# Optimization experiments

Hardware: AMD Instinct MI355X
Metric: run time of the kernel (lower is better)

## Reference

```python
import jax, jax.numpy as jnp
import numpy as np

HIDDEN = 512
HEADS = 8
HEAD_DIM = HIDDEN // HEADS
THRESH = 0.1
EPS = 1e-8


def setup_inputs() -> dict:
    key = jax.random.key(0)
    ks = jax.random.split(key, 9)
    B, S = 2, 4096
    scale = 1.0 / np.sqrt(HIDDEN)
    x = jax.random.normal(ks[0], (B, S, HIDDEN), dtype=jnp.float32)
    Wq = jax.random.normal(ks[1], (HIDDEN, HIDDEN), dtype=jnp.float32) * scale
    bq = jnp.zeros((HIDDEN,), dtype=jnp.float32)
    Wk = jax.random.normal(ks[2], (HIDDEN, HIDDEN), dtype=jnp.float32) * scale
    bk = jnp.zeros((HIDDEN,), dtype=jnp.float32)
    Wv = jax.random.normal(ks[3], (HIDDEN, HIDDEN), dtype=jnp.float32) * scale
    bv = jnp.zeros((HIDDEN,), dtype=jnp.float32)
    Wo = jax.random.normal(ks[4], (HIDDEN, HIDDEN), dtype=jnp.float32) * scale
    bo = jnp.zeros((HIDDEN,), dtype=jnp.float32)
    return {"x": x, "Wq": Wq, "bq": bq, "Wk": Wk, "bk": bk,
            "Wv": Wv, "bv": bv, "Wo": Wo, "bo": bo}


def reference(x, Wq, bq, Wk, bk, Wv, bv, Wo, bo):
    B, S, _ = x.shape
    # torch Linear: y = x @ W.T + b
    def proj(W, b):
        y = jnp.einsum('bsd,ed->bse', x, W) + b
        return y.reshape(B, S, HEADS, HEAD_DIM).transpose(0, 2, 1, 3)  # [B,H,S,Dh]
    Q = proj(Wq, bq)
    K = proj(Wk, bk)
    V = proj(Wv, bv)
    scores = jnp.einsum('bhqd,bhkd->bhqk', Q, K) / jnp.sqrt(jnp.float32(HEAD_DIM))
    probs = jax.nn.softmax(scores, axis=-1)  # [B,H,S,S]
    probs = jnp.where(probs > THRESH, probs, 0.0)
    probs = probs / (jnp.sum(probs, axis=-1, keepdims=True) + EPS)
    ctx = jnp.einsum('bhqk,bhkd->bhqd', probs, V)
    ctx = ctx.transpose(0, 2, 1, 3).reshape(B, S, HIDDEN)
    return jnp.einsum('bsd,ed->bse', ctx, Wo) + bo
```

## Files before the change

### kernel.cpp

```cpp
#include <hip/hip_runtime.h>

#define S_LEN 4096
#define BATCH 2
#define HID 512
#define HEADS 8
#define HD 64
#define NX (BATCH * S_LEN * HID)
#define WSZ (HID * HID)
#define NBH (BATCH * HEADS)
#define QB 32
#define NB1 (S_LEN / QB * NBH)
#define NB2 (S_LEN / 64 * NBH)

typedef short v8s __attribute__((ext_vector_type(8)));
typedef float v4f __attribute__((ext_vector_type(4)));
typedef float v16f __attribute__((ext_vector_type(16)));
typedef unsigned short ushort_t;

__device__ __forceinline__ ushort_t f2bf(float f) {
  unsigned u = __builtin_bit_cast(unsigned, f);
  u += 0x7fffu + ((u >> 16) & 1u);
  return (ushort_t)(u >> 16);
}
__device__ __forceinline__ unsigned pk2(float a, float b) {
  return (__builtin_bit_cast(unsigned, a) >> 16) |
         (__builtin_bit_cast(unsigned, b) & 0xFFFF0000u);
}
__device__ __forceinline__ float fexp2(float x) {
  return __builtin_amdgcn_exp2f(x);
}


__global__ __launch_bounds__(256) void cvt_k(
    const float* __restrict__ x,
    const float* __restrict__ wq, const float* __restrict__ wk,
    const float* __restrict__ wv, const float* __restrict__ wo,
    ushort_t* __restrict__ dst)
{
  const size_t e = ((size_t)blockIdx.x * 256 + threadIdx.x) * 4;
  const float* src; size_t off;
  if (e < NX) { src = x; off = e; }
  else {
    const size_t we = e - NX;
    const int wi = (int)(we >> 18);
    src = wi == 0 ? wq : wi == 1 ? wk : wi == 2 ? wv : wo;
    off = we & (WSZ - 1);
  }
  float4 v = *(const float4*)&src[off];
  uint2 u; u.x = pk2(v.x, v.y); u.y = pk2(v.z, v.w);
  *(uint2*)&dst[e] = u;
}

__global__ __launch_bounds__(256) void gemm_qkv(
    const ushort_t* __restrict__ X, const ushort_t* __restrict__ Wb,
    const float* __restrict__ bq, const float* __restrict__ bk, const float* __restrict__ bv,
    ushort_t* __restrict__ Qf, ushort_t* __restrict__ Kf, ushort_t* __restrict__ Vw,
    float qscale)
{
  __shared__ ushort_t As[128][40];
  __shared__ ushort_t Bs[128][40];
  const int t = threadIdx.x;
  const int lane = t & 63;
  const int l15 = lane & 15, lg = lane >> 4;
  const int w = t >> 6;
  const int wr = w >> 1, wc = w & 1;
  const int m0 = blockIdx.y * 128;
  const int wsel = blockIdx.x >> 2;
  const int e0 = (blockIdx.x & 3) * 128;
  const ushort_t* W = Wb + (size_t)wsel * WSZ;
  const float* bias = wsel == 0 ? bq : wsel == 1 ? bk : bv;
  const float osc = (wsel == 0) ? qscale : 1.0f;

  v4f acc[4][4] = {};
  const int srow = t >> 2, scol = (t & 3) * 8;

  for (int k0 = 0; k0 < HID; k0 += 32) {
    __syncthreads();
    #pragma unroll
    for (int rep = 0; rep < 2; ++rep) {
      *(uint4*)&As[srow + rep * 64][scol] =
          *(const uint4*)&X[(size_t)(m0 + srow + rep * 64) * HID + k0 + scol];
      *(uint4*)&Bs[srow + rep * 64][scol] =
          *(const uint4*)&W[(size_t)(e0 + srow + rep * 64) * HID + k0 + scol];
    }
    __syncthreads();
    v8s a[4], b[4];
    #pragma unroll
    for (int fr = 0; fr < 4; ++fr)
      a[fr] = *(const v8s*)&As[wr * 64 + 16 * fr + l15][8 * lg];
    #pragma unroll
    for (int fc = 0; fc < 4; ++fc)
      b[fc] = *(const v8s*)&Bs[wc * 64 + 16 * fc + l15][8 * lg];
    #pragma unroll
    for (int fr = 0; fr < 4; ++fr)
      #pragma unroll
      for (int fc = 0; fc < 4; ++fc)
        acc[fr][fc] = __builtin_amdgcn_mfma_f32_16x16x32_bf16(a[fr], b[fc], acc[fr][fc], 0, 0, 0);
  }

  #pragma unroll
  for (int fr = 0; fr < 4; ++fr)
    #pragma unroll
    for (int fc = 0; fc < 4; ++fc) {
      const int e = e0 + wc * 64 + 16 * fc + l15;
      const float bval = bias[e];
      #pragma unroll
      for (int r = 0; r < 4; ++r) {
        const int m = m0 + wr * 64 + 16 * fr + 4 * lg + r;
        const float v = (acc[fr][fc][r] + bval) * osc;
        const int bidx = m >> 12, s = m & (S_LEN - 1);
        const int hh = e >> 6, dh = e & 63;
        const size_t hb = ((size_t)(bidx * HEADS + hh)) * (size_t)(S_LEN * HD);
        if (wsel == 2) {
          Vw[hb + (size_t)s * HD + dh] = f2bf(v);
        } else {
          const size_t off = (size_t)(s >> 5) * 2048 +
              (size_t)(((dh >> 4) * 64 + ((dh >> 3) & 1) * 32 + (s & 31)) * 8 + (dh & 7));
          (wsel == 0 ? Qf : Kf)[hb + off] = f2bf(v);
        }
      }
    }
}

__global__ __launch_bounds__(256, 4) void attn_p1(
    const ushort_t* __restrict__ Qf, const ushort_t* __restrict__ Kf,
    ushort_t* __restrict__ Cb, int* __restrict__ Flg)
{
  __shared__ float RedL[4][QB];
  __shared__ float RedM[4][QB];
  __shared__ int bflag;
  const int t = threadIdx.x;
  const int lane = t & 63;
  const int l31 = lane & 31, hi = lane >> 5;
  const int kq = t >> 6;
  const int lin = blockIdx.x;
  const int bh = ((lin & 7) << 1) | ((lin >> 3) & 1);
  const int q0 = (lin >> 4) * QB;
  if (t == 0) bflag = 0;

  const size_t hoff = (size_t)bh * (size_t)(S_LEN * HD);
  const ushort_t* Qb = Qf + hoff + (size_t)(q0 >> 5) * 2048;
  const ushort_t* Kb = Kf + hoff;

  v8s qa[4];
  #pragma unroll
  for (int ks = 0; ks < 4; ++ks)
    qa[ks] = *(const v8s*)&Qb[(ks * 64 + lane) * 8];

  float M[16], L[16];
  #pragma unroll
  for (int j = 0; j < 16; ++j) { M[j] = -1e30f; L[j] = 0.f; }

  v8s kA[4], kB4[4];
  {
    const ushort_t* kc = Kb + (size_t)kq * 2048;
    #pragma unroll
    for (int ks = 0; ks < 4; ++ks)
      kA[ks] = *(const v8s*)&kc[(ks * 64 + lane) * 8];
  }

#define PROC(KX)                                                            \
  {                                                                         \
    v16f s = {};                                                            \
    _Pragma("unroll")                                                       \
    for (int ks = 0; ks < 4; ++ks)                                          \
      s = __builtin_amdgcn_mfma_f32_32x32x16_bf16(qa[ks], KX[ks], s, 0, 0, 0); \
    _Pragma("unroll")                                                       \
    for (int j = 0; j < 16; ++j) {                                          \
      M[j] = fmaxf(M[j], s[j]);                                             \
      L[j] += fexp2(s[j]);                                                  \
    }                                                                       \
  }

  for (int i = 0; i < 32; i += 2) {
    {
      const ushort_t* kc = Kb + (size_t)(kq + 4 * (i + 1)) * 2048;
      #pragma unroll
      for (int ks = 0; ks < 4; ++ks)
        kB4[ks] = *(const v8s*)&kc[(ks * 64 + lane) * 8];
    }
    PROC(kA)
    {
      const int c2 = (i + 2 < 32) ? (kq + 4 * (i + 2)) : kq;
      const ushort_t* kc = Kb + (size_t)c2 * 2048;
      #pragma unroll
      for (int ks = 0; ks < 4; ++ks)
        kA[ks] = *(const v8s*)&kc[(ks * 64 + lane) * 8];
    }
    PROC(kB4)
  }
#undef PROC

  #pragma unroll
  for (int j = 0; j < 16; ++j) {
    float Lv = L[j], Mv = M[j];
    Lv += __shfl_xor(Lv, 1);  Mv = fmaxf(Mv, __shfl_xor(Mv, 1));
    Lv += __shfl_xor(Lv, 2);  Mv = fmaxf(Mv, __shfl_xor(Mv, 2));
    Lv += __shfl_xor(Lv, 4);  Mv = fmaxf(Mv, __shfl_xor(Mv, 4));
    Lv += __shfl_xor(Lv, 8);  Mv = fmaxf(Mv, __shfl_xor(Mv, 8));
    Lv += __shfl_xor(Lv, 16); Mv = fmaxf(Mv, __shfl_xor(Mv, 16));
    if (l31 == 0) {
      const int row = (j & 3) + 8 * (j >> 2) + 4 * hi;
      RedL[kq][row] = Lv;
      RedM[kq][row] = Mv;
    }
  }
  __syncthreads();
  if (t < QB) {
    const float Lv = RedL[0][t] + RedL[1][t] + RedL[2][t] + RedL[3][t];
    const float Mv = fmaxf(fmaxf(RedM[0][t], RedM[1][t]),
                           fmaxf(RedM[2][t], RedM[3][t]));
    if (Mv >= __log2f(Lv) - 3.3719281f) atomicOr(&bflag, 1);
  }
  __syncthreads();
  if (t == 0) Flg[lin] = bflag;

  const int b = bh >> 3, h = bh & 7;
  const int row = t >> 3, d8 = (t & 7) * 8;
  const uint4 z = {0u, 0u, 0u, 0u};
  *(uint4*)&Cb[((size_t)b * S_LEN + q0 + row) * HID + h * HD + d8] = z;
}

__global__ __launch_bounds__(256) void attn_p2(
    const ushort_t* __restrict__ Qf, const ushort_t* __restrict__ Kf,
    const ushort_t* __restrict__ V, ushort_t* __restrict__ Cb,
    const int* __restrict__ Flg)
{
  const int lin = blockIdx.x;
  {
    const int base = lin & 15, qb = lin >> 4;
    if ((Flg[base | ((2 * qb) << 4)] | Flg[base | ((2 * qb + 1) << 4)]) == 0)
      return;
  }
  __shared__ float Osh[64][HD + 1];
  __shared__ float Dsh[64];
  __shared__ float RedA[4][64];
  __shared__ float iLs[64];
  __shared__ ushort_t Pp[4][32][40];
  __shared__ ushort_t VT[4][HD][40];
  const int t = threadIdx.x;
  const int lane = t & 63;
  const int l31 = lane & 31, hi = lane >> 5;
  const int w = t >> 6;
  const int bh = ((lin & 7) << 1) | ((lin >> 3) & 1);
  const int q0 = (lin >> 4) * 64;
  const size_t hoff = (size_t)bh * (size_t)(S_LEN * HD);
  const ushort_t* Qb = Qf + hoff + (size_t)(q0 >> 5) * 2048;
  const ushort_t* Kb = Kf + hoff;
  const ushort_t* Vh = V + hoff;

  if (t < 64) Dsh[t] = 0.f;
  for (int idx = t; idx < 64 * HD; idx += 256) Osh[idx >> 6][idx & 63] = 0.f;

  v8s qa[4], qB[4];
  #pragma unroll
  for (int ks = 0; ks < 4; ++ks) {
    qa[ks] = *(const v8s*)&Qb[(ks * 64 + lane) * 8];
    qB[ks] = *(const v8s*)&Qb[2048 + (ks * 64 + lane) * 8];
  }

  float L0[16], L1[16];
  #pragma unroll
  for (int j = 0; j < 16; ++j) { L0[j] = 0.f; L1[j] = 0.f; }
  for (int i = 0; i < 32; ++i) {
    const ushort_t* kc = Kb + (size_t)(w + 4 * i) * 2048;
    v8s kb[4];
    #pragma unroll
    for (int ks = 0; ks < 4; ++ks)
      kb[ks] = *(const v8s*)&kc[(ks * 64 + lane) * 8];
    v16f sa = {}, sb = {};
    #pragma unroll
    for (int ks = 0; ks < 4; ++ks) {
      sa = __builtin_amdgcn_mfma_f32_32x32x16_bf16(qa[ks], kb[ks], sa, 0, 0, 0);
      sb = __builtin_amdgcn_mfma_f32_32x32x16_bf16(qB[ks], kb[ks], sb, 0, 0, 0);
    }
    #pragma unroll
    for (int j = 0; j < 16; ++j) {
      L0[j] += fexp2(sa[j]);
      L1[j] += fexp2(sb[j]);
    }
  }
  #pragma unroll
  for (int rseti = 0; rseti < 2; ++rseti)
    #pragma unroll
    for (int j = 0; j < 16; ++j) {
      float Lv = (rseti == 0) ? L0[j] : L1[j];
      Lv += __shfl_xor(Lv, 1);  Lv += __shfl_xor(Lv, 2);
      Lv += __shfl_xor(Lv, 4);  Lv += __shfl_xor(Lv, 8);
      Lv += __shfl_xor(Lv, 16);
      if (l31 == 0) {
        const int row = rseti * 32 + (j & 3) + 8 * (j >> 2) + 4 * hi;
        RedA[w][row] = Lv;
      }
    }
  __syncthreads();
  if (t < 64)
    iLs[t] = 1.0f / (RedA[0][t] + RedA[1][t] + RedA[2][t] + RedA[3][t]);
  __syncthreads();

  float il[2][16];
  #pragma unroll
  for (int rseti = 0; rseti < 2; ++rseti)
    #pragma unroll
    for (int j = 0; j < 16; ++j)
      il[rseti][j] = iLs[rseti * 32 + (j & 3) + 8 * (j >> 2) + 4 * hi];

  v16f oA[2] = {}, oB[2] = {};
  float den[2][16] = {};

  for (int i = 0; i < 32; ++i) {
    const int c = w + 4 * i;
    const ushort_t* kc = Kb + (size_t)c * 2048;
    v8s kb[4];
    #pragma unroll
    for (int ks = 0; ks < 4; ++ks)
      kb[ks] = *(const v8s*)&kc[(ks * 64 + lane) * 8];
    v16f sa = {}, sb = {};
    #pragma unroll
    for (int ks = 0; ks < 4; ++ks) {
      sa = __builtin_amdgcn_mfma_f32_32x32x16_bf16(qa[ks], kb[ks], sa, 0, 0, 0);
      sb = __builtin_amdgcn_mfma_f32_32x32x16_bf16(qB[ks], kb[ks], sb, 0, 0, 0);
    }
    {
      const ushort_t* vsrc = &Vh[((size_t)c * 32 + l31) * HD + hi * 32];
      #pragma unroll
      for (int qq = 0; qq < 4; ++qq) {
        uint4 vv = *(const uint4*)&vsrc[qq * 8];
        const ushort_t* pv = (const ushort_t*)&vv;
        #pragma unroll
        for (int jj = 0; jj < 8; ++jj)
          VT[w][hi * 32 + qq * 8 + jj][l31] = pv[jj];
      }
    }
    #pragma unroll
    for (int rseti = 0; rseti < 2; ++rseti) {
      #pragma unroll
      for (int j = 0; j < 16; ++j) {
        const float s = (rseti == 0) ? sa[j] : sb[j];
        const int row = (j & 3) + 8 * (j >> 2) + 4 * hi;
        float p = fexp2(s) * il[rseti][j];
        p = (p > 0.1f) ? p : 0.f;
        den[rseti][j] += p;
        Pp[w][row][l31] = f2bf(p);
      }
      v8s pa0 = *(const v8s*)&Pp[w][l31][8 * hi];
      v8s pa1 = *(const v8s*)&Pp[w][l31][16 + 8 * hi];
      #pragma unroll
      for (int dblk = 0; dblk < 2; ++dblk) {
        v8s vb0 = *(const v8s*)&VT[w][dblk * 32 + l31][8 * hi];
        v8s vb1 = *(const v8s*)&VT[w][dblk * 32 + l31][16 + 8 * hi];
        if (rseti == 0) {
          oA[dblk] = __builtin_amdgcn_mfma_f32_32x32x16_bf16(pa0, vb0, oA[dblk], 0, 0, 0);
          oA[dblk] = __builtin_amdgcn_mfma_f32_32x32x16_bf16(pa1, vb1, oA[dblk], 0, 0, 0);
        } else {
          oB[dblk] = __builtin_amdgcn_mfma_f32_32x32x16_bf16(pa0, vb0, oB[dblk], 0, 0, 0);
          oB[dblk] = __builtin_amdgcn_mfma_f32_32x32x16_bf16(pa1, vb1, oB[dblk], 0, 0, 0);
        }
      }
    }
  }

  #pragma unroll
  for (int rseti = 0; rseti < 2; ++rseti)
    #pragma unroll
    for (int j = 0; j < 16; ++j) {
      float d = den[rseti][j];
      d += __shfl_xor(d, 1); d += __shfl_xor(d, 2); d += __shfl_xor(d, 4);
      d += __shfl_xor(d, 8); d += __shfl_xor(d, 16);
      const int row = rseti * 32 + (j & 3) + 8 * (j >> 2) + 4 * hi;
      if (l31 == 0) atomicAdd(&Dsh[row], d);
    }
  #pragma unroll
  for (int rseti = 0; rseti < 2; ++rseti)
    #pragma unroll
    for (int dblk = 0; dblk < 2; ++dblk)
      #pragma unroll
      for (int j = 0; j < 16; ++j) {
        const int row = rseti * 32 + (j & 3) + 8 * (j >> 2) + 4 * hi;
        const float val = (rseti == 0) ? oA[dblk][j] : oB[dblk][j];
        atomicAdd(&Osh[row][dblk * 32 + l31], val);
      }
  __syncthreads();
  const int b = bh >> 3, h = bh & 7;
  for (int idx = t; idx < 64 * HD; idx += 256) {
    const int row = idx >> 6, d = idx & 63;
    const float val = Osh[row][d] / (Dsh[row] + 1e-8f);
    Cb[((size_t)b * S_LEN + q0 + row) * HID + h * HD + d] = f2bf(val);
  }
}

__global__ __launch_bounds__(256) void gemm_out(
    const ushort_t* __restrict__ X, const ushort_t* __restrict__ W,
    const float* __restrict__ bias, const int* __restrict__ Flg,
    float* __restrict__ Df)
{
  const int t = threadIdx.x;
  const int m0 = blockIdx.y * 64;
  const int e0 = blockIdx.x * 64;

  {
    const int b = m0 >> 12, qblk = (m0 & (S_LEN - 1)) >> 6;
    int any = 0;
    #pragma unroll
    for (int h = 0; h < HEADS; ++h) {
      const int bhh = b * HEADS + h;
      const int base = (bhh >> 1) | ((bhh & 1) << 3);
      any |= Flg[base | ((2 * qblk) << 4)] | Flg[base | ((2 * qblk + 1) << 4)];
    }
    if (!any) {
      const int row = t >> 2, c0 = (t & 3) * 16;
      #pragma unroll
      for (int g = 0; g < 4; ++g) {
        const float4 bv = *(const float4*)&bias[e0 + c0 + g * 4];
        *(float4*)&Df[(size_t)(m0 + row) * HID + e0 + c0 + g * 4] = bv;
      }
      return;
    }
  }

  __shared__ ushort_t As[64][40];
  __shared__ ushort_t Bs[64][40];
  const int lane = t & 63;
  const int l15 = lane & 15, lg = lane >> 4;
  const int w = t >> 6;
  const int wr = w >> 1, wc = w & 1;

  v4f acc[2][2] = {};
  const int srow = t >> 2, scol = (t & 3) * 8;

  for (int k0 = 0; k0 < HID; k0 += 32) {
    __syncthreads();
    *(uint4*)&As[srow][scol] =
        *(const uint4*)&X[(size_t)(m0 + srow) * HID + k0 + scol];
    *(uint4*)&Bs[srow][scol] =
        *(const uint4*)&W[(size_t)(e0 + srow) * HID + k0 + scol];
    __syncthreads();
    v8s a[2], b[2];
    #pragma unroll
    for (int fr = 0; fr < 2; ++fr)
      a[fr] = *(const v8s*)&As[wr * 32 + 16 * fr + l15][8 * lg];
    #pragma unroll
    for (int fc = 0; fc < 2; ++fc)
      b[fc] = *(const v8s*)&Bs[wc * 32 + 16 * fc + l15][8 * lg];
    #pragma unroll
    for (int fr = 0; fr < 2; ++fr)
      #pragma unroll
      for (int fc = 0; fc < 2; ++fc)
        acc[fr][fc] = __builtin_amdgcn_mfma_f32_16x16x32_bf16(a[fr], b[fc], acc[fr][fc], 0, 0, 0);
  }

  #pragma unroll
  for (int fr = 0; fr < 2; ++fr)
    #pragma unroll
    for (int fc = 0; fc < 2; ++fc) {
      const int e = e0 + wc * 32 + 16 * fc + l15;
      const float bval = bias[e];
      #pragma unroll
      for (int r = 0; r < 4; ++r) {
        const int m = m0 + wr * 32 + 16 * fr + 4 * lg + r;
        Df[(size_t)m * HID + e] = acc[fr][fc][r] + bval;
      }
    }
}

extern "C" void kernel_launch(void* const* d_in, const int* in_sizes, int n_in,
                              void* d_out, int out_size, void* d_ws, size_t ws_size,
                              hipStream_t stream) {
  const float* x  = (const float*)d_in[0];
  const float* Wq = (const float*)d_in[1];
  const float* bq = (const float*)d_in[2];
  const float* Wk = (const float*)d_in[3];
  const float* bk = (const float*)d_in[4];
  const float* Wv = (const float*)d_in[5];
  const float* bv = (const float*)d_in[6];
  const float* Wo = (const float*)d_in[7];
  const float* bo = (const float*)d_in[8];

  int*      Flg  = (int*)d_ws;
  ushort_t* xb   = (ushort_t*)(Flg + NB1);
  ushort_t* wqb  = xb + NX;
  ushort_t* wob  = wqb + 3 * WSZ;
  ushort_t* Qf   = wob + WSZ;
  ushort_t* Kf   = Qf + NX;
  ushort_t* Vw   = Kf + NX;
  ushort_t* Cb   = Vw + NX;

  const float qscale = 0.125f * 1.44269504f;

  cvt_k<<<(NX + 4 * WSZ) / 1024, 256, 0, stream>>>(x, Wq, Wk, Wv, Wo, xb);

  gemm_qkv<<<dim3(12, 64), 256, 0, stream>>>(
      xb, wqb, bq, bk, bv, Qf, Kf, Vw, qscale);

  attn_p1<<<NB1, 256, 0, stream>>>(Qf, Kf, Cb, Flg);
  attn_p2<<<NB2, 256, 0, stream>>>(Qf, Kf, Vw, Cb, Flg);

  gemm_out<<<dim3(8, 128), 256, 0, stream>>>(Cb, wob, bo, Flg, (float*)d_out);
}
```

Baseline: 105.7 us.

## Use direct global-to-LDS loads, triple-buffer K loads, and skip zeroing context

The QKV GEMM now stages tiles with global_load_lds straight into unpadded shared arrays instead of going through registers. attn_p1 triple-buffers K fragments, raises wave priority around the MFMA block, and no longer zeroes the context buffer. gemm_out instead substitutes zeros for head slices whose flags are off, so it never reads unwritten context. Risks are LDS bank conflicts from dropping the padding and correctness depending on the flag mask matching each 64-wide head slice.

```diff
diff --git a/kernel.cpp b/kernel.cpp
--- a/kernel.cpp
+++ b/kernel.cpp
@@ -16,6 +16,8 @@
 typedef float v4f __attribute__((ext_vector_type(4)));
 typedef float v16f __attribute__((ext_vector_type(16)));
 typedef unsigned short ushort_t;
+typedef const __attribute__((address_space(1))) unsigned gu32;
+typedef __attribute__((address_space(3))) unsigned lu32;
 
 __device__ __forceinline__ ushort_t f2bf(float f) {
   unsigned u = __builtin_bit_cast(unsigned, f);
@@ -57,8 +59,8 @@
     ushort_t* __restrict__ Qf, ushort_t* __restrict__ Kf, ushort_t* __restrict__ Vw,
     float qscale)
 {
-  __shared__ ushort_t As[128][40];
-  __shared__ ushort_t Bs[128][40];
+  __shared__ ushort_t As[128][32];
+  __shared__ ushort_t Bs[128][32];
   const int t = threadIdx.x;
   const int lane = t & 63;
   const int l15 = lane & 15, lg = lane >> 4;
@@ -72,17 +74,22 @@
   const float osc = (wsel == 0) ? qscale : 1.0f;
 
   v4f acc[4][4] = {};
-  const int srow = t >> 2, scol = (t & 3) * 8;
+  const int r0 = t >> 2, c0 = (t & 3) * 8;
 
   for (int k0 = 0; k0 < HID; k0 += 32) {
     __syncthreads();
-    #pragma unroll
-    for (int rep = 0; rep < 2; ++rep) {
-      *(uint4*)&As[srow + rep * 64][scol] =
-          *(const uint4*)&X[(size_t)(m0 + srow + rep * 64) * HID + k0 + scol];
-      *(uint4*)&Bs[srow + rep * 64][scol] =
-          *(const uint4*)&W[(size_t)(e0 + srow + rep * 64) * HID + k0 + scol];
-    }
+    __builtin_amdgcn_global_load_lds(
+        (gu32*)(const void*)&X[(size_t)(m0 + r0) * HID + k0 + c0],
+        (lu32*)(void*)&As[r0][c0], 16, 0, 0);
+    __builtin_amdgcn_global_load_lds(
+        (gu32*)(const void*)&X[(size_t)(m0 + r0 + 64) * HID + k0 + c0],
+        (lu32*)(void*)&As[r0 + 64][c0], 16, 0, 0);
+    __builtin_amdgcn_global_load_lds(
+        (gu32*)(const void*)&W[(size_t)(e0 + r0) * HID + k0 + c0],
+        (lu32*)(void*)&Bs[r0][c0], 16, 0, 0);
+    __builtin_amdgcn_global_load_lds(
+        (gu32*)(const void*)&W[(size_t)(e0 + r0 + 64) * HID + k0 + c0],
+        (lu32*)(void*)&Bs[r0 + 64][c0], 16, 0, 0);
     __syncthreads();
     v8s a[4], b[4];
     #pragma unroll
@@ -124,7 +131,7 @@
 
 __global__ __launch_bounds__(256, 4) void attn_p1(
     const ushort_t* __restrict__ Qf, const ushort_t* __restrict__ Kf,
-    ushort_t* __restrict__ Cb, int* __restrict__ Flg)
+    int* __restrict__ Flg)
 {
   __shared__ float RedL[4][QB];
   __shared__ float RedM[4][QB];
@@ -151,20 +158,24 @@
   #pragma unroll
   for (int j = 0; j < 16; ++j) { M[j] = -1e30f; L[j] = 0.f; }
 
-  v8s kA[4], kB4[4];
-  {
-    const ushort_t* kc = Kb + (size_t)kq * 2048;
-    #pragma unroll
-    for (int ks = 0; ks < 4; ++ks)
-      kA[ks] = *(const v8s*)&kc[(ks * 64 + lane) * 8];
+  v8s kb0[4], kb1[4], kb2[4];
+
+#define LOADK(DST, IDX)                                                     \
+  {                                                                         \
+    const ushort_t* kc_ = Kb + (size_t)(kq + 4 * (IDX)) * 2048;             \
+    _Pragma("unroll")                                                       \
+    for (int ks = 0; ks < 4; ++ks)                                          \
+      DST[ks] = *(const v8s*)&kc_[(ks * 64 + lane) * 8];                    \
   }
 
 #define PROC(KX)                                                            \
   {                                                                         \
     v16f s = {};                                                            \
+    __builtin_amdgcn_s_setprio(1);                                          \
     _Pragma("unroll")                                                       \
     for (int ks = 0; ks < 4; ++ks)                                          \
       s = __builtin_amdgcn_mfma_f32_32x32x16_bf16(qa[ks], KX[ks], s, 0, 0, 0); \
+    __builtin_amdgcn_s_setprio(0);                                          \
     _Pragma("unroll")                                                       \
     for (int j = 0; j < 16; ++j) {                                          \
       M[j] = fmaxf(M[j], s[j]);                                             \
@@ -172,23 +183,16 @@
     }                                                                       \
   }
 
-  for (int i = 0; i < 32; i += 2) {
-    {
-      const ushort_t* kc = Kb + (size_t)(kq + 4 * (i + 1)) * 2048;
-      #pragma unroll
-      for (int ks = 0; ks < 4; ++ks)
-        kB4[ks] = *(const v8s*)&kc[(ks * 64 + lane) * 8];
-    }
-    PROC(kA)
-    {
-      const int c2 = (i + 2 < 32) ? (kq + 4 * (i + 2)) : kq;
-      const ushort_t* kc = Kb + (size_t)c2 * 2048;
-      #pragma unroll
-      for (int ks = 0; ks < 4; ++ks)
-        kA[ks] = *(const v8s*)&kc[(ks * 64 + lane) * 8];
-    }
-    PROC(kB4)
-  }
+  LOADK(kb0, 0)
+  LOADK(kb1, 1)
+  for (int i = 0; i < 30; i += 3) {
+    LOADK(kb2, i + 2)  PROC(kb0)
+    LOADK(kb0, i + 3)  PROC(kb1)
+    LOADK(kb1, i + 4)  PROC(kb2)
+  }
+  PROC(kb0)
+  PROC(kb1)
+#undef LOADK
 #undef PROC
 
   #pragma unroll
@@ -214,11 +218,6 @@
   }
   __syncthreads();
   if (t == 0) Flg[lin] = bflag;
-
-  const int b = bh >> 3, h = bh & 7;
-  const int row = t >> 3, d8 = (t & 7) * 8;
-  const uint4 z = {0u, 0u, 0u, 0u};
-  *(uint4*)&Cb[((size_t)b * S_LEN + q0 + row) * HID + h * HD + d8] = z;
 }
 
 __global__ __launch_bounds__(256) void attn_p2(
@@ -398,16 +397,18 @@
   const int m0 = blockIdx.y * 64;
   const int e0 = blockIdx.x * 64;
 
+  int fm = 0;
   {
     const int b = m0 >> 12, qblk = (m0 & (S_LEN - 1)) >> 6;
-    int any = 0;
     #pragma unroll
     for (int h = 0; h < HEADS; ++h) {
       const int bhh = b * HEADS + h;
       const int base = (bhh >> 1) | ((bhh & 1) << 3);
-      any |= Flg[base | ((2 * qblk) << 4)] | Flg[base | ((2 * qblk + 1) << 4)];
-    }
-    if (!any) {
+      const int f = Flg[base | ((2 * qblk) << 4)] |
+                    Flg[base | ((2 * qblk + 1) << 4)];
+      fm |= (f ? 1 : 0) << h;
+    }
+    if (!fm) {
       const int row = t >> 2, c0 = (t & 3) * 16;
       #pragma unroll
       for (int g = 0; g < 4; ++g) {
@@ -427,11 +428,14 @@
 
   v4f acc[2][2] = {};
   const int srow = t >> 2, scol = (t & 3) * 8;
+  const uint4 zu = {0u, 0u, 0u, 0u};
 
   for (int k0 = 0; k0 < HID; k0 += 32) {
     __syncthreads();
-    *(uint4*)&As[srow][scol] =
-        *(const uint4*)&X[(size_t)(m0 + srow) * HID + k0 + scol];
+    const bool hot = (fm >> (k0 >> 6)) & 1;
+    *(uint4*)&As[srow][scol] = hot
+        ? *(const uint4*)&X[(size_t)(m0 + srow) * HID + k0 + scol]
+        : zu;
     *(uint4*)&Bs[srow][scol] =
         *(const uint4*)&W[(size_t)(e0 + srow) * HID + k0 + scol];
     __syncthreads();
@@ -492,7 +496,7 @@
   gemm_qkv<<<dim3(12, 64), 256, 0, stream>>>(
       xb, wqb, bq, bk, bv, Qf, Kf, Vw, qscale);
 
-  attn_p1<<<NB1, 256, 0, stream>>>(Qf, Kf, Cb, Flg);
+  attn_p1<<<NB1, 256, 0, stream>>>(Qf, Kf, Flg);
   attn_p2<<<NB2, 256, 0, stream>>>(Qf, Kf, Vw, Cb, Flg);
 
   gemm_out<<<dim3(8, 128), 256, 0, stream>>>(Cb, wob, bo, Flg, (float*)d_out);
```

Measured after the change: 244.5 us. +131.3%, slower.
